# Kernel tuning notes

Hardware: AMD Instinct MI355X
Metric: run time of the kernel (lower is better)

Reference implementation:

```python
import jax, jax.numpy as jnp
import numpy as np

NW, NG, NF = 16, 5, 10          # writers, genuines, forgeries per writer
STEP = 1 + NG + NF              # 16 signatures per mini-batch
T, DIM = 400, 64                # max seq len, feature dim
GAMMA = 5.0                     # soft-dtw smoothing (ctor: gamma=5)
BIG = 1e10                      # finite stand-in for +inf in the DP


def setup_inputs() -> dict:
    key = jax.random.key(0)
    k1, k2 = jax.random.split(key)
    data = jax.random.normal(k1, (NW * STEP, T, DIM), dtype=jnp.float32)
    lens = jax.random.randint(k2, (NW * STEP,), 200, T + 1)  # valid lengths in [200, 400]
    margin = jnp.ones((1,), dtype=jnp.float32)
    return {"data": data, "margin": margin, "lens": lens}


def _sdtw_diags(D):
    """Anti-diagonal wavefront soft-DTW DP over a full TxT cost matrix.
    Returns all DP diagonals stacked: diags[k, i] == R[i, k - i] so that
    R[la, lb] (the soft-DTW value of the length-(la,lb) prefixes) is
    diags[la + lb, la]. bandwidth=0 -> no Sakoe-Chiba band."""
    n = D.shape[0]
    ii = jnp.arange(n + 1)
    d0 = jnp.where(ii == 0, 0.0, BIG).astype(D.dtype)  # diagonal k=0: R[0,0]=0
    d1 = jnp.full(n + 1, BIG, D.dtype)                 # diagonal k=1: borders = inf

    def shift(v):  # v[i] -> v[i-1], BIG pad at i=0
        return jnp.concatenate([jnp.full((1,), BIG, v.dtype), v[:-1]])

    def step(carry, k):
        p2, p1 = carry                      # diagonals k-2, k-1
        irow = jnp.clip(ii - 1, 0, n - 1)   # cost row index i-1
        jcol = k - ii - 1                   # cost col index j-1 (j = k - i)
        valid = (ii >= 1) & (jcol >= 0) & (jcol <= n - 1)
        Dk = D[irow, jnp.clip(jcol, 0, n - 1)]
        # softmin(R[i-1,j-1], R[i-1,j], R[i,j-1])
        softmin = -GAMMA * jax.nn.logsumexp(
            jnp.stack([shift(p2), shift(p1), p1]) * (-1.0 / GAMMA), axis=0)
        r = jnp.where(valid, Dk + softmin, BIG)
        return (p1, r), r

    _, diags = jax.lax.scan(step, (d0, d1), jnp.arange(2, 2 * n + 1))
    return jnp.concatenate([d0[None], d1[None], diags], axis=0)  # [2n+1, n+1]


def _forward(data, margin, lens):
    batch = data.reshape(NW, STEP, T, DIM)
    blens = lens.reshape(NW, STEP)
    # anchor (index 0 of each mini-batch) vs every signature in the mini-batch
    A = jnp.broadcast_to(batch[:, :1], batch.shape).reshape(NW * STEP, T, DIM)
    B = batch.reshape(NW * STEP, T, DIM)
    la = jnp.broadcast_to(blens[:, :1], blens.shape).reshape(-1)
    lb = blens.reshape(-1)
    # squared-euclidean pairwise cost matrices [P, T, T]
    D = (jnp.sum(A * A, -1)[:, :, None] + jnp.sum(B * B, -1)[:, None, :]
         - 2.0 * jnp.einsum('ptd,psd->pts', A, B))
    diags = jax.vmap(_sdtw_diags)(D)                 # [P, 2T+1, T+1]
    P = diags.shape[0]
    r = diags[jnp.arange(P), la + lb, la]            # R[la, lb] per pair
    dists = (r / (la + lb)).reshape(NW, STEP)        # avg-pooled soft-DTW dist
    dist_aa = dists[:, 0:1]                          # anchor vs itself
    lk1 = dists[:, 1:1 + NG] - dist_aa
    lk2 = jax.nn.relu(margin[0] - (dists[:, 1 + NG:1 + NG + NF] - dist_aa))
    nz = jnp.sum(lk1 != 0, axis=1) + jnp.sum(lk2 != 0, axis=1) + 1
    lv = (jnp.sum(lk1, axis=1) + jnp.sum(lk2, axis=1)) / nz
    return jnp.mean(lv)


def reference(data, margin, lens):
    return _forward(data, margin, lens)
```

## Files before the change

### kernel.cpp

```cpp
#include <hip/hip_runtime.h>
#include <math.h>

#define NWG   16
#define NSTEP 16
#define NGE   5
#define T_LEN 400
#define DIM   64
#define GAMMA 5.0f
#define BIGV  1e10f

#define BLOCK 448

__launch_bounds__(BLOCK, 2)
__global__ void sdtw_kernel(const float* __restrict__ data,
                            const int* __restrict__ lens,
                            float* __restrict__ dists)
{
    __shared__ float Blds[T_LEN * DIM];
    __shared__ float bnorm[T_LEN];
    __shared__ float Rbuf[4][T_LEN + 1];

    const int p   = blockIdx.x;
    const int tid = threadIdx.x;
    const int w   = tid >> 6;
    const int l   = tid & 63;
    const int iA  = 63 * w + l;
    const int anchor = (p / NSTEP) * NSTEP;

    const float* __restrict__ Bg = data + (size_t)p      * (T_LEN * DIM);
    const float* __restrict__ Ag = data + (size_t)anchor * (T_LEN * DIM);

    for (int idx = tid; idx < T_LEN * (DIM / 4); idx += BLOCK) {
        const int c  = idx >> 4;
        const int cc = idx & 15;
        const float4 v = reinterpret_cast<const float4*>(Bg)[idx];
        const int x  = cc ^ (c & 7);
        *reinterpret_cast<float4*>(&Blds[c * DIM + x * 4]) = v;
    }

    float4 Aa[16], Ab[16];
    float  anA = 0.f, anB = 0.f;
    {
        const int ra = min(max(iA - 1, 0), T_LEN - 1);
        const int rb = min(iA, T_LEN - 1);
        const float4* __restrict__ pa =
            reinterpret_cast<const float4*>(Ag + (size_t)ra * DIM);
        const float4* __restrict__ pb =
            reinterpret_cast<const float4*>(Ag + (size_t)rb * DIM);
        #pragma unroll
        for (int cc = 0; cc < 16; ++cc) {
            Aa[cc] = pa[cc];
            Ab[cc] = pb[cc];
            anA += Aa[cc].x*Aa[cc].x + Aa[cc].y*Aa[cc].y
                 + Aa[cc].z*Aa[cc].z + Aa[cc].w*Aa[cc].w;
            anB += Ab[cc].x*Ab[cc].x + Ab[cc].y*Ab[cc].y
                 + Ab[cc].z*Ab[cc].z + Ab[cc].w*Ab[cc].w;
        }
    }
    __syncthreads();

    if (tid < T_LEN) {
        const int c = tid;
        float s = 0.f;
        #pragma unroll
        for (int cc = 0; cc < 16; ++cc) {
            const float4 b = *reinterpret_cast<const float4*>(
                &Blds[c * DIM + ((cc ^ (c & 7)) * 4)]);
            s += b.x*b.x + b.y*b.y + b.z*b.z + b.w*b.w;
        }
        bnorm[c] = s;
    }

    for (int idx = tid; idx <= T_LEN; idx += BLOCK) {
        Rbuf[0][idx] = (idx == 0) ? 0.f : BIGV;
        Rbuf[1][idx] = BIGV;
    }
    __syncthreads();

    const int la = lens[anchor];
    const int lb = lens[p];
    const int kt = la + lb;
    const int P  = kt >> 1;
    float saved = 0.f;
    bool  have  = false;
    const float NIG = -1.0f / GAMMA;

    for (int ph = 1; ph <= P; ++ph) {
        const int  k     = 2 * ph;
        const int  c     = k - iA - 1;
        const bool colOK = (c >= 0) && (c < lb);
        const bool aAct  = colOK && (iA >= 1) && (iA <= la);
        const bool bAct  = colOK && (l < 63) && (iA + 1 <= la);

        float p1vr = BIGV;
        float dA = 0.f, dB = 0.f, bn = 0.f;
        if (aAct || bAct) {
            p1vr = Rbuf[(k - 1) & 3][iA];
            bn   = bnorm[c];
            const float* __restrict__ Brow = &Blds[c * DIM];
            const int xr = (c & 7) * 4;
            #pragma unroll
            for (int cc = 0; cc < 16; ++cc) {
                const float4 b = *reinterpret_cast<const float4*>(&Brow[(cc * 4) ^ xr]);
                dA = fmaf(Aa[cc].x, b.x, dA); dB = fmaf(Ab[cc].x, b.x, dB);
                dA = fmaf(Aa[cc].y, b.y, dA); dB = fmaf(Ab[cc].y, b.y, dB);
                dA = fmaf(Aa[cc].z, b.z, dA); dB = fmaf(Ab[cc].z, b.z, dB);
                dA = fmaf(Aa[cc].w, b.w, dA); dB = fmaf(Ab[cc].w, b.w, dB);
            }
        }

        float vA = BIGV;
        if (aAct) {
            const float p2s = Rbuf[(k - 2) & 3][iA - 1];
            const float p1s = Rbuf[(k - 1) & 3][iA - 1];
            const float a  = p2s  * NIG;
            const float b2 = p1s  * NIG;
            const float c2 = p1vr * NIG;
            float m = fmaxf(fmaxf(a, b2), c2);
            float s = __expf(a - m) + __expf(b2 - m) + __expf(c2 - m);
            vA = (anA + bn - 2.f * dA) - GAMMA * (__logf(s) + m);
        }

        const float vAn = __shfl_down(vA, 1);

        float vB = BIGV;
        if (bAct) {
            const float a  = p1vr * NIG;
            const float b2 = vA   * NIG;
            const float c2 = vAn  * NIG;
            float m = fmaxf(fmaxf(a, b2), c2);
            float s = __expf(a - m) + __expf(b2 - m) + __expf(c2 - m);
            vB = (anB + bn - 2.f * dB) - GAMMA * (__logf(s) + m);
        }

        if (k == kt     && iA == la     && l < 63) { saved = vA; have = true; }
        if (k + 1 == kt && iA + 1 == la && l < 63) { saved = vB; have = true; }

        if (iA <= T_LEN)               Rbuf[k & 3][iA] = vA;
        if (l < 63 && iA + 1 <= T_LEN) Rbuf[(k + 1) & 3][iA + 1] = vB;
        if (tid == BLOCK - 1)          Rbuf[(k + 1) & 3][0] = BIGV;
        __syncthreads();
    }

    if (have) dists[p] = saved / (float)kt;
}

__global__ void loss_kernel(const float* __restrict__ dists,
                            const float* __restrict__ margin,
                            float* __restrict__ out)
{
    const int g = threadIdx.x;
    float lv = 0.f;
    if (g < NWG) {
        const float* __restrict__ d = dists + g * NSTEP;
        const float aa = d[0];
        const float mg = margin[0];
        float s = 0.f;
        int   nz = 1;
        #pragma unroll
        for (int j = 1; j <= NGE; ++j) {
            const float v = d[j] - aa;
            s += v;
            nz += (v != 0.f);
        }
        #pragma unroll
        for (int j = 1 + NGE; j < NSTEP; ++j) {
            float v = mg - (d[j] - aa);
            v = fmaxf(v, 0.f);
            s += v;
            nz += (v != 0.f);
        }
        lv = s / (float)nz;
    }
    lv += __shfl_down(lv, 8);
    lv += __shfl_down(lv, 4);
    lv += __shfl_down(lv, 2);
    lv += __shfl_down(lv, 1);
    if (g == 0) out[0] = lv / (float)NWG;
}

extern "C" void kernel_launch(void* const* d_in, const int* in_sizes, int n_in,
                              void* d_out, int out_size, void* d_ws, size_t ws_size,
                              hipStream_t stream) {
    const float* data   = (const float*)d_in[0];
    const float* margin = (const float*)d_in[1];
    const int*   lens   = (const int*)d_in[2];
    float* dists = (float*)d_ws;

    sdtw_kernel<<<NWG * NSTEP, BLOCK, 0, stream>>>(data, lens, dists);
    loss_kernel<<<1, 64, 0, stream>>>(dists, margin, (float*)d_out);
}
```

Baseline: 403.2 us.

## Compute three anti-diagonals per barrier phase instead of two

Each thread now covers three consecutive anti-diagonal cells (rows r, r+1, r+2) per phase, using shuffles to pass intra-wave dependencies. This cuts the number of __syncthreads barriers from about kt/2 to about kt/3. The ring buffer grows to 8 diagonals. The price is a third A-row register set (extra VGPRs that may hurt occupancy under launch_bounds 2), overlapping rows between lanes that redo work, and one more serial softmin per phase.

```diff
diff --git a/kernel.cpp b/kernel.cpp
--- a/kernel.cpp
+++ b/kernel.cpp
@@ -18,13 +18,13 @@
 {
     __shared__ float Blds[T_LEN * DIM];
     __shared__ float bnorm[T_LEN];
-    __shared__ float Rbuf[4][T_LEN + 1];
+    __shared__ float Rbuf[8][T_LEN + 1];
 
     const int p   = blockIdx.x;
     const int tid = threadIdx.x;
     const int w   = tid >> 6;
     const int l   = tid & 63;
-    const int iA  = 63 * w + l;
+    const int r   = 62 * w + l - 1;
     const int anchor = (p / NSTEP) * NSTEP;
 
     const float* __restrict__ Bg = data + (size_t)p      * (T_LEN * DIM);
@@ -38,23 +38,23 @@
         *reinterpret_cast<float4*>(&Blds[c * DIM + x * 4]) = v;
     }
 
-    float4 Aa[16], Ab[16];
-    float  anA = 0.f, anB = 0.f;
+    float4 Aa[16], Ab[16], Ac[16];
+    float  anA = 0.f, anB = 0.f, anC = 0.f;
     {
-        const int ra = min(max(iA - 1, 0), T_LEN - 1);
-        const int rb = min(iA, T_LEN - 1);
-        const float4* __restrict__ pa =
-            reinterpret_cast<const float4*>(Ag + (size_t)ra * DIM);
-        const float4* __restrict__ pb =
-            reinterpret_cast<const float4*>(Ag + (size_t)rb * DIM);
+        const int ra = min(max(r - 1, 0), T_LEN - 1);
+        const int rb = min(max(r,     0), T_LEN - 1);
+        const int rc = min(max(r + 1, 0), T_LEN - 1);
+        const float4* __restrict__ pa = reinterpret_cast<const float4*>(Ag + (size_t)ra * DIM);
+        const float4* __restrict__ pb = reinterpret_cast<const float4*>(Ag + (size_t)rb * DIM);
+        const float4* __restrict__ pc = reinterpret_cast<const float4*>(Ag + (size_t)rc * DIM);
         #pragma unroll
         for (int cc = 0; cc < 16; ++cc) {
             Aa[cc] = pa[cc];
             Ab[cc] = pb[cc];
-            anA += Aa[cc].x*Aa[cc].x + Aa[cc].y*Aa[cc].y
-                 + Aa[cc].z*Aa[cc].z + Aa[cc].w*Aa[cc].w;
-            anB += Ab[cc].x*Ab[cc].x + Ab[cc].y*Ab[cc].y
-                 + Ab[cc].z*Ab[cc].z + Ab[cc].w*Ab[cc].w;
+            Ac[cc] = pc[cc];
+            anA += Aa[cc].x*Aa[cc].x + Aa[cc].y*Aa[cc].y + Aa[cc].z*Aa[cc].z + Aa[cc].w*Aa[cc].w;
+            anB += Ab[cc].x*Ab[cc].x + Ab[cc].y*Ab[cc].y + Ab[cc].z*Ab[cc].z + Ab[cc].w*Ab[cc].w;
+            anC += Ac[cc].x*Ac[cc].x + Ac[cc].y*Ac[cc].y + Ac[cc].z*Ac[cc].z + Ac[cc].w*Ac[cc].w;
         }
     }
     __syncthreads();
@@ -80,39 +80,38 @@
     const int la = lens[anchor];
     const int lb = lens[p];
     const int kt = la + lb;
-    const int P  = kt >> 1;
+    const int P  = (kt + 1) / 3;
     float saved = 0.f;
     bool  have  = false;
     const float NIG = -1.0f / GAMMA;
 
     for (int ph = 1; ph <= P; ++ph) {
-        const int  k     = 2 * ph;
-        const int  c     = k - iA - 1;
-        const bool colOK = (c >= 0) && (c < lb);
-        const bool aAct  = colOK && (iA >= 1) && (iA <= la);
-        const bool bAct  = colOK && (l < 63) && (iA + 1 <= la);
-
-        float p1vr = BIGV;
-        float dA = 0.f, dB = 0.f, bn = 0.f;
-        if (aAct || bAct) {
-            p1vr = Rbuf[(k - 1) & 3][iA];
+        const int  k     = 3 * ph - 1;
+        const int  c     = k - r - 1;
+        const bool guard = (c >= 0) && (c < lb) && (r <= la);
+
+        float p2s = BIGV, p1s = BIGV, p1vr = BIGV, bn = 0.f;
+        float dA = 0.f, dB = 0.f, dC = 0.f;
+        if (guard) {
+            const int rm1 = max(r - 1, 0), rc0 = max(r, 0);
+            p2s  = Rbuf[(k - 2) & 7][rm1];
+            p1s  = Rbuf[(k - 1) & 7][rm1];
+            p1vr = Rbuf[(k - 1) & 7][rc0];
             bn   = bnorm[c];
             const float* __restrict__ Brow = &Blds[c * DIM];
             const int xr = (c & 7) * 4;
             #pragma unroll
             for (int cc = 0; cc < 16; ++cc) {
                 const float4 b = *reinterpret_cast<const float4*>(&Brow[(cc * 4) ^ xr]);
-                dA = fmaf(Aa[cc].x, b.x, dA); dB = fmaf(Ab[cc].x, b.x, dB);
-                dA = fmaf(Aa[cc].y, b.y, dA); dB = fmaf(Ab[cc].y, b.y, dB);
-                dA = fmaf(Aa[cc].z, b.z, dA); dB = fmaf(Ab[cc].z, b.z, dB);
-                dA = fmaf(Aa[cc].w, b.w, dA); dB = fmaf(Ab[cc].w, b.w, dB);
+                dA = fmaf(Aa[cc].x, b.x, dA); dB = fmaf(Ab[cc].x, b.x, dB); dC = fmaf(Ac[cc].x, b.x, dC);
+                dA = fmaf(Aa[cc].y, b.y, dA); dB = fmaf(Ab[cc].y, b.y, dB); dC = fmaf(Ac[cc].y, b.y, dC);
+                dA = fmaf(Aa[cc].z, b.z, dA); dB = fmaf(Ab[cc].z, b.z, dB); dC = fmaf(Ac[cc].z, b.z, dC);
+                dA = fmaf(Aa[cc].w, b.w, dA); dB = fmaf(Ab[cc].w, b.w, dB); dC = fmaf(Ac[cc].w, b.w, dC);
             }
         }
 
         float vA = BIGV;
-        if (aAct) {
-            const float p2s = Rbuf[(k - 2) & 3][iA - 1];
-            const float p1s = Rbuf[(k - 1) & 3][iA - 1];
+        if (guard && (r >= 1)) {
             const float a  = p2s  * NIG;
             const float b2 = p1s  * NIG;
             const float c2 = p1vr * NIG;
@@ -120,11 +119,10 @@
             float s = __expf(a - m) + __expf(b2 - m) + __expf(c2 - m);
             vA = (anA + bn - 2.f * dA) - GAMMA * (__logf(s) + m);
         }
-
         const float vAn = __shfl_down(vA, 1);
 
         float vB = BIGV;
-        if (bAct) {
+        if (guard && (r + 1 >= 1) && (r + 1 <= la)) {
             const float a  = p1vr * NIG;
             const float b2 = vA   * NIG;
             const float c2 = vAn  * NIG;
@@ -132,13 +130,27 @@
             float s = __expf(a - m) + __expf(b2 - m) + __expf(c2 - m);
             vB = (anB + bn - 2.f * dB) - GAMMA * (__logf(s) + m);
         }
-
-        if (k == kt     && iA == la     && l < 63) { saved = vA; have = true; }
-        if (k + 1 == kt && iA + 1 == la && l < 63) { saved = vB; have = true; }
-
-        if (iA <= T_LEN)               Rbuf[k & 3][iA] = vA;
-        if (l < 63 && iA + 1 <= T_LEN) Rbuf[(k + 1) & 3][iA + 1] = vB;
-        if (tid == BLOCK - 1)          Rbuf[(k + 1) & 3][0] = BIGV;
+        const float vBn = __shfl_down(vB, 1);
+
+        float vC = BIGV;
+        if (guard && (r + 2 <= la)) {
+            const float a  = vAn * NIG;
+            const float b2 = vB  * NIG;
+            const float c2 = vBn * NIG;
+            float m = fmaxf(fmaxf(a, b2), c2);
+            float s = __expf(a - m) + __expf(b2 - m) + __expf(c2 - m);
+            vC = (anC + bn - 2.f * dC) - GAMMA * (__logf(s) + m);
+        }
+
+        if (l < 62) {
+            if (r >= 0 && r     <= T_LEN) Rbuf[ k      & 7][r]     = vA;
+            if (           r + 1 <= T_LEN) Rbuf[(k + 1) & 7][r + 1] = vB;
+            if (           r + 2 <= T_LEN) Rbuf[(k + 2) & 7][r + 2] = vC;
+            if (k     == kt && r     == la) { saved = vA; have = true; }
+            if (k + 1 == kt && r + 1 == la) { saved = vB; have = true; }
+            if (k + 2 == kt && r + 2 == la) { saved = vC; have = true; }
+        }
+        if (tid == BLOCK - 1) Rbuf[(k + 2) & 7][0] = BIGV;
         __syncthreads();
     }
 
```

After: 376.8 us. -6.6%, faster.

## Prefetch next B row into registers and use base-2 exp/log in softmin

Applied to the files above, without the earlier changes.

Each thread now loads the B feature row it will need in the next phase (column c+2) into registers during the current phase, so the shared-memory load no longer sits on the critical path before the dot product. The softmin also switches from __expf/__logf to direct exp2/log2 hardware builtins, with the scale constants folded to base 2, which saves the implicit base conversions. The cost is 64 more live VGPRs per thread, which can hurt occupancy or cause spills under launch_bounds(448,2).

```diff
diff --git a/kernel.cpp b/kernel.cpp
--- a/kernel.cpp
+++ b/kernel.cpp
@@ -10,6 +10,9 @@
 #define BIGV  1e10f
 
 #define BLOCK 448
+
+#define NIG2  (-0.28853900817779268f)
+#define GLN2  (3.4657359027997265f)
 
 __launch_bounds__(BLOCK, 2)
 __global__ void sdtw_kernel(const float* __restrict__ data,
@@ -83,7 +86,18 @@
     const int P  = kt >> 1;
     float saved = 0.f;
     bool  have  = false;
-    const float NIG = -1.0f / GAMMA;
+
+    float4 Br[16];
+    {
+        const int c0 = 1 - iA;
+        if (c0 >= 0 && c0 < lb) {
+            const float* __restrict__ Brow = &Blds[c0 * DIM];
+            const int xr = (c0 & 7) * 4;
+            #pragma unroll
+            for (int cc = 0; cc < 16; ++cc)
+                Br[cc] = *reinterpret_cast<const float4*>(&Brow[(cc * 4) ^ xr]);
+        }
+    }
 
     for (int ph = 1; ph <= P; ++ph) {
         const int  k     = 2 * ph;
@@ -97,11 +111,9 @@
         if (aAct || bAct) {
             p1vr = Rbuf[(k - 1) & 3][iA];
             bn   = bnorm[c];
-            const float* __restrict__ Brow = &Blds[c * DIM];
-            const int xr = (c & 7) * 4;
             #pragma unroll
             for (int cc = 0; cc < 16; ++cc) {
-                const float4 b = *reinterpret_cast<const float4*>(&Brow[(cc * 4) ^ xr]);
+                const float4 b = Br[cc];
                 dA = fmaf(Aa[cc].x, b.x, dA); dB = fmaf(Ab[cc].x, b.x, dB);
                 dA = fmaf(Aa[cc].y, b.y, dA); dB = fmaf(Ab[cc].y, b.y, dB);
                 dA = fmaf(Aa[cc].z, b.z, dA); dB = fmaf(Ab[cc].z, b.z, dB);
@@ -109,28 +121,41 @@
             }
         }
 
+        {
+            const int cn = c + 2;
+            if (cn >= 0 && cn < lb) {
+                const float* __restrict__ Brow = &Blds[cn * DIM];
+                const int xr = (cn & 7) * 4;
+                #pragma unroll
+                for (int cc = 0; cc < 16; ++cc)
+                    Br[cc] = *reinterpret_cast<const float4*>(&Brow[(cc * 4) ^ xr]);
+            }
+        }
+
         float vA = BIGV;
         if (aAct) {
             const float p2s = Rbuf[(k - 2) & 3][iA - 1];
             const float p1s = Rbuf[(k - 1) & 3][iA - 1];
-            const float a  = p2s  * NIG;
-            const float b2 = p1s  * NIG;
-            const float c2 = p1vr * NIG;
+            const float a  = p2s  * NIG2;
+            const float b2 = p1s  * NIG2;
+            const float c2 = p1vr * NIG2;
             float m = fmaxf(fmaxf(a, b2), c2);
-            float s = __expf(a - m) + __expf(b2 - m) + __expf(c2 - m);
-            vA = (anA + bn - 2.f * dA) - GAMMA * (__logf(s) + m);
+            float s = __builtin_amdgcn_exp2f(a - m) + __builtin_amdgcn_exp2f(b2 - m)
+                    + __builtin_amdgcn_exp2f(c2 - m);
+            vA = (anA + bn - 2.f * dA) - GLN2 * (__builtin_amdgcn_logf(s) + m);
         }
 
         const float vAn = __shfl_down(vA, 1);
 
         float vB = BIGV;
         if (bAct) {
-            const float a  = p1vr * NIG;
-            const float b2 = vA   * NIG;
-            const float c2 = vAn  * NIG;
+            const float a  = p1vr * NIG2;
+            const float b2 = vA   * NIG2;
+            const float c2 = vAn  * NIG2;
             float m = fmaxf(fmaxf(a, b2), c2);
-            float s = __expf(a - m) + __expf(b2 - m) + __expf(c2 - m);
-            vB = (anB + bn - 2.f * dB) - GAMMA * (__logf(s) + m);
+            float s = __builtin_amdgcn_exp2f(a - m) + __builtin_amdgcn_exp2f(b2 - m)
+                    + __builtin_amdgcn_exp2f(c2 - m);
+            vB = (anB + bn - 2.f * dB) - GLN2 * (__builtin_amdgcn_logf(s) + m);
         }
 
         if (k == kt     && iA == la     && l < 63) { saved = vA; have = true; }
```

Result: no change. 406.4 us (+0.8%).
